# Kernel optimization log

Hardware: AMD Instinct MI355X
Metric: run time of the kernel (lower is better)

The kernel has to match this reference:

```python
import jax, jax.numpy as jnp
import numpy as np

NUM_USERS, NUM_ITEMS, D = 100000, 200000, 128
B, LLEN, SLEN = 4096, 200, 50
NEG = -1e9


def setup_inputs() -> dict:
    key = jax.random.key(0)
    ks = jax.random.split(key, 10)
    w_range = float(np.sqrt(3.0 / D))
    return {
        "user_table": 0.01 * jax.random.normal(ks[0], (NUM_USERS, D), dtype=jnp.float32),
        "item_table": 0.01 * jax.random.normal(ks[1], (NUM_ITEMS, D), dtype=jnp.float32),
        "W1": jax.random.uniform(ks[2], (2 * D, 16), minval=-w_range, maxval=w_range, dtype=jnp.float32),
        "b1": jnp.zeros((16,), dtype=jnp.float32),
        "W2": jax.random.uniform(ks[3], (16, 1), minval=-w_range, maxval=w_range, dtype=jnp.float32),
        "b2": jnp.zeros((1,), dtype=jnp.float32),
        "user_inputs": jax.random.randint(ks[4], (B,), 0, NUM_USERS, dtype=jnp.int64) if jax.config.jax_enable_x64 else jax.random.randint(ks[4], (B,), 0, NUM_USERS, dtype=jnp.int32),
        "L_inputs": jax.random.randint(ks[5], (B, LLEN), 0, NUM_ITEMS, dtype=jnp.int32),
        "S_inputs": jax.random.randint(ks[6], (B, SLEN), 0, NUM_ITEMS, dtype=jnp.int32),
        "item_inputs": jax.random.randint(ks[7], (B,), 0, NUM_ITEMS, dtype=jnp.int32),
    }


def reference(user_table, item_table, W1, b1, W2, b2,
              user_inputs, L_inputs, S_inputs, item_inputs):
    def att_logits(x):  # x: [..., 2D] -> [...]
        h = jax.nn.relu(x @ W1 + b1)
        return (h @ W2 + b2)[..., 0]

    def masked_softmax(logits, mask):  # softmax over last axis restricted to mask
        logits = jnp.where(mask, logits, NEG)
        return jax.nn.softmax(logits, axis=-1)

    u_emb = user_table[user_inputs]                      # [B, D]

    # ---- long-term attention over L history ----
    L_mask = L_inputs >= 0                               # [B, L]
    L_idx = jnp.where(L_mask, L_inputs, 0)
    L_emb = item_table[L_idx]                            # [B, L, D]
    uL = jnp.concatenate([jnp.broadcast_to(u_emb[:, None, :], L_emb.shape), L_emb], axis=-1)  # [B, L, 2D]
    w1 = masked_softmax(att_logits(uL), L_mask)          # [B, L]
    u_long = jnp.einsum('bl,bld->bd', w1, L_emb)         # [B, D]

    # ---- short-term attention over [u_long] + S (L assumed nonempty) ----
    S_mask = S_inputs >= 0                               # [B, S]
    S_idx = jnp.where(S_mask, S_inputs, 0)
    S_emb = item_table[S_idx]                            # [B, S, D]
    seq = jnp.concatenate([u_long[:, None, :], S_emb], axis=1)   # [B, 1+S, D]
    seq_mask = jnp.concatenate([jnp.ones((seq.shape[0], 1), dtype=bool), S_mask], axis=1)
    uSeq = jnp.concatenate([jnp.broadcast_to(u_emb[:, None, :], seq.shape), seq], axis=-1)  # [B, 1+S, 2D]
    w2 = masked_softmax(att_logits(uSeq), seq_mask)      # [B, 1+S]
    user_hybrid = jnp.einsum('bs,bsd->bd', w2, seq)      # [B, D]

    # ---- score: bmm([B,1,D], [B,D,1]) -> [B,1,1] ----
    item_emb = item_table[item_inputs]                   # [B, D]
    score = jnp.sum(user_hybrid * item_emb, axis=-1)[:, None, None]
    return score
```

## Files before the change

kernel.cpp:

```cpp
#include <hip/hip_runtime.h>
#include <math.h>

#define D 128
#define LLEN 200
#define SLEN 50
#define CH 64
#define ESTR 129
#define NEG (-1e9f)

__device__ __forceinline__ float wave_red_sum(float v) {
#pragma unroll
  for (int m = 32; m >= 1; m >>= 1) v += __shfl_xor(v, m, 64);
  return v;
}
__device__ __forceinline__ float block_sum(float v, float* red) {
  v = wave_red_sum(v);
  if ((threadIdx.x & 63) == 0) red[threadIdx.x >> 6] = v;
  __syncthreads();
  v = red[0] + red[1] + red[2] + red[3];
  __syncthreads();
  return v;
}

__global__ void __launch_bounds__(256, 4) din_kernel(
    const float* __restrict__ user_table, const float* __restrict__ item_table,
    const float* __restrict__ W1, const float* __restrict__ b1,
    const float* __restrict__ W2, const float* __restrict__ b2,
    const int* __restrict__ user_inputs, const int* __restrict__ L_inputs,
    const int* __restrict__ S_inputs, const int* __restrict__ item_inputs,
    float* __restrict__ out) {
  __shared__ float ebuf[CH * ESTR];
  __shared__ float hspart[4 * 65];
  __shared__ float w_sh[CH];
  __shared__ int rows1[LLEN];
  __shared__ int rowsS[SLEN];
  __shared__ float upart_sh[16];
  __shared__ float red_sh[4];

  const int b = blockIdx.x;
  const int tid = threadIdx.x;
  const int lane = tid & 63;
  const int w = __builtin_amdgcn_readfirstlane(tid >> 6);
  const int dd = tid & 127, dg = tid >> 7;
  const float4* it4 = reinterpret_cast<const float4*>(item_table);

  float* u_sh = &ebuf[0];
  float* part = &ebuf[128];
  if (tid < D) u_sh[tid] = user_table[(size_t)user_inputs[b] * D + tid];
  if (tid < LLEN) rows1[tid] = L_inputs[(size_t)b * LLEN + tid];
  if (tid < SLEN) rowsS[tid] = S_inputs[(size_t)b * SLEN + tid];
  __syncthreads();

  {
    int j = tid & 15, g = tid >> 4;
    float p = 0.f;
#pragma unroll
    for (int t = 0; t < 8; ++t) {
      int d = g * 8 + t;
      p = fmaf(u_sh[d], W1[d * 16 + j], p);
    }
    part[tid] = p;
  }
  __syncthreads();
  if (tid < 16) {
    float s = b1[tid];
#pragma unroll
    for (int g = 0; g < 16; ++g) s += part[g * 16 + tid];
    upart_sh[tid] = s;
  }
  __syncthreads();

  const float b2v = b2[0];
  const float w2a = W2[4 * w + 0], w2b = W2[4 * w + 1];
  const float w2c = W2[4 * w + 2], w2d = W2[4 * w + 3];

  float pacc = 0.f;
  float uacc = 0.f;

  for (int c = 0; c < 4; ++c) {
    const int base = c * CH;
    const int cnt = (base + CH <= LLEN) ? CH : (LLEN - base);
    const int nslot = cnt * 32;

    {
      float4 v[8];
#pragma unroll
      for (int it = 0; it < 8; ++it) {
        int s = tid + it * 256;
        if (s < nslot) {
          int gid = rows1[base + (s >> 5)];
          if (gid < 0) gid = 0;
          v[it] = it4[(size_t)gid * 32 + (s & 31)];
        }
      }
#pragma unroll
      for (int it = 0; it < 8; ++it) {
        int s = tid + it * 256;
        if (s < nslot) {
          float* dst = &ebuf[(s >> 5) * ESTR + 4 * (s & 31)];
          dst[0] = v[it].x; dst[1] = v[it].y; dst[2] = v[it].z; dst[3] = v[it].w;
        }
      }
    }
    __syncthreads();

    if (lane < cnt) {
      float a0 = 0.f, a1 = 0.f, a2 = 0.f, a3 = 0.f;
      const float* er = &ebuf[lane * ESTR];
      const float* wc = &W1[(size_t)D * 16 + 4 * w];
#pragma unroll 16
      for (int d = 0; d < D; ++d) {
        float e = er[d];
        const float* wr = wc + d * 16;
        a0 = fmaf(e, wr[0], a0);
        a1 = fmaf(e, wr[1], a1);
        a2 = fmaf(e, wr[2], a2);
        a3 = fmaf(e, wr[3], a3);
      }
      float hs = fmaxf(upart_sh[4 * w + 0] + a0, 0.f) * w2a;
      hs = fmaf(fmaxf(upart_sh[4 * w + 1] + a1, 0.f), w2b, hs);
      hs = fmaf(fmaxf(upart_sh[4 * w + 2] + a2, 0.f), w2c, hs);
      hs = fmaf(fmaxf(upart_sh[4 * w + 3] + a3, 0.f), w2d, hs);
      hspart[w * 65 + lane] = hs;
    }
    __syncthreads();

    if (tid < cnt) {
      float lg = hspart[tid] + hspart[65 + tid] + hspart[130 + tid] +
                 hspart[195 + tid] + b2v;
      float p = (rows1[base + tid] >= 0) ? expf(lg) : 0.f;
      w_sh[tid] = p;
      pacc += p;
    }
    __syncthreads();

    for (int l = dg; l < cnt; l += 2)
      uacc = fmaf(w_sh[l], ebuf[l * ESTR + dd], uacc);
    __syncthreads();
  }

  const float invS1 = 1.f / block_sum(pacc, red_sh);
  float* part2 = &ebuf[60 * ESTR];
  part2[tid] = uacc;
  __syncthreads();
  if (tid < D) {
    float ul = (part2[tid] + part2[tid + D]) * invS1;
    ebuf[tid] = ul;
  }
  __syncthreads();

  {
    const int nslot = SLEN * 32;
    float4 v[7];
#pragma unroll
    for (int it = 0; it < 7; ++it) {
      int s = tid + it * 256;
      if (s < nslot) {
        int gid = rowsS[s >> 5];
        if (gid < 0) gid = 0;
        v[it] = it4[(size_t)gid * 32 + (s & 31)];
      }
    }
#pragma unroll
    for (int it = 0; it < 7; ++it) {
      int s = tid + it * 256;
      if (s < nslot) {
        float* dst = &ebuf[((s >> 5) + 1) * ESTR + 4 * (s & 31)];
        dst[0] = v[it].x; dst[1] = v[it].y; dst[2] = v[it].z; dst[3] = v[it].w;
      }
    }
  }
  __syncthreads();

  const int n2 = 1 + SLEN;
  if (lane < n2) {
    float a0 = 0.f, a1 = 0.f, a2 = 0.f, a3 = 0.f;
    const float* er = &ebuf[lane * ESTR];
    const float* wc = &W1[(size_t)D * 16 + 4 * w];
#pragma unroll 16
    for (int d = 0; d < D; ++d) {
      float e = er[d];
      const float* wr = wc + d * 16;
      a0 = fmaf(e, wr[0], a0);
      a1 = fmaf(e, wr[1], a1);
      a2 = fmaf(e, wr[2], a2);
      a3 = fmaf(e, wr[3], a3);
    }
    float hs = fmaxf(upart_sh[4 * w + 0] + a0, 0.f) * w2a;
    hs = fmaf(fmaxf(upart_sh[4 * w + 1] + a1, 0.f), w2b, hs);
    hs = fmaf(fmaxf(upart_sh[4 * w + 2] + a2, 0.f), w2c, hs);
    hs = fmaf(fmaxf(upart_sh[4 * w + 3] + a3, 0.f), w2d, hs);
    hspart[w * 65 + lane] = hs;
  }
  __syncthreads();

  float p2 = 0.f;
  if (tid < n2) {
    float lg = hspart[tid] + hspart[65 + tid] + hspart[130 + tid] +
               hspart[195 + tid] + b2v;
    bool valid = (tid == 0) || (rowsS[tid - 1] >= 0);
    p2 = valid ? expf(lg) : 0.f;
    w_sh[tid] = p2;
  }
  const float invS2 = 1.f / block_sum(p2, red_sh);

  float uacc2 = 0.f;
  for (int l = dg; l < n2; l += 2)
    uacc2 = fmaf(w_sh[l], ebuf[l * ESTR + dd], uacc2);
  part2[tid] = uacc2;
  __syncthreads();

  float sv = 0.f;
  if (tid < D) {
    float uh = (part2[tid] + part2[tid + D]) * invS2;
    sv = uh * item_table[(size_t)item_inputs[b] * D + tid];
  }
  float tot = block_sum(sv, red_sh);
  if (tid == 0) out[b] = tot;
}

extern "C" void kernel_launch(void* const* d_in, const int* in_sizes, int n_in,
                              void* d_out, int out_size, void* d_ws, size_t ws_size,
                              hipStream_t stream) {
  const float* user_table = (const float*)d_in[0];
  const float* item_table = (const float*)d_in[1];
  const float* W1 = (const float*)d_in[2];
  const float* b1 = (const float*)d_in[3];
  const float* W2 = (const float*)d_in[4];
  const float* b2 = (const float*)d_in[5];
  const int* user_inputs = (const int*)d_in[6];
  const int* L_inputs = (const int*)d_in[7];
  const int* S_inputs = (const int*)d_in[8];
  const int* item_inputs = (const int*)d_in[9];
  float* out = (float*)d_out;

  const int B = in_sizes[6];
  din_kernel<<<B, 256, 0, stream>>>(user_table, item_table, W1, b1, W2, b2,
                                    user_inputs, L_inputs, S_inputs, item_inputs,
                                    out);
}
```

Baseline: 294.9 us.

## Prefetch next history chunk into registers and vectorize LDS access with float4

The gather of each 64-row chunk of the long history is now issued before the weighted-sum phase of the previous chunk, and the short-sequence gather is issued before the first softmax reduction. The goal is to hide global gather latency behind compute. The row stride is padded to 132 so rows are 16-byte aligned in shared memory, which lets LDS stores, the MLP dot products and the weighted sums all use float4 accesses. The weighted sum also moves from 2 to 8 row groups, with an 8-way final reduction. In exchange the kernel keeps 32 extra VGPRs of prefetched data live, which may hurt occupancy under the 256x4 launch bound, and the padded stride may change bank-conflict behaviour.

```diff
diff --git a/kernel.cpp b/kernel.cpp
--- a/kernel.cpp
+++ b/kernel.cpp
@@ -5,7 +5,7 @@
 #define LLEN 200
 #define SLEN 50
 #define CH 64
-#define ESTR 129
+#define ESTR 132
 #define NEG (-1e9f)
 
 __device__ __forceinline__ float wave_red_sum(float v) {
@@ -41,7 +41,8 @@
   const int tid = threadIdx.x;
   const int lane = tid & 63;
   const int w = __builtin_amdgcn_readfirstlane(tid >> 6);
-  const int dd = tid & 127, dg = tid >> 7;
+  const int col4 = tid & 31;
+  const int grp  = tid >> 5;
   const float4* it4 = reinterpret_cast<const float4*>(item_table);
 
   float* u_sh = &ebuf[0];
@@ -51,6 +52,23 @@
   if (tid < SLEN) rowsS[tid] = S_inputs[(size_t)b * SLEN + tid];
   __syncthreads();
 
+  auto load_chunk = [&](float4 (&v)[8], int c) {
+    const int base = c * CH;
+    const int cnt = (base + CH <= LLEN) ? CH : (LLEN - base);
+    const int nslot = cnt * 32;
+#pragma unroll
+    for (int it = 0; it < 8; ++it) {
+      int s = tid + it * 256;
+      if (s < nslot) {
+        int gid = rows1[base + (s >> 5)];
+        if (gid < 0) gid = 0;
+        v[it] = it4[(size_t)gid * 32 + (s & 31)];
+      }
+    }
+  };
+  float4 v[8];
+  load_chunk(v, 0);
+
   {
     int j = tid & 15, g = tid >> 4;
     float p = 0.f;
@@ -75,47 +93,37 @@
   const float w2c = W2[4 * w + 2], w2d = W2[4 * w + 3];
 
   float pacc = 0.f;
-  float uacc = 0.f;
+  float4 uacc = make_float4(0.f, 0.f, 0.f, 0.f);
 
   for (int c = 0; c < 4; ++c) {
     const int base = c * CH;
     const int cnt = (base + CH <= LLEN) ? CH : (LLEN - base);
     const int nslot = cnt * 32;
 
-    {
-      float4 v[8];
-#pragma unroll
-      for (int it = 0; it < 8; ++it) {
-        int s = tid + it * 256;
-        if (s < nslot) {
-          int gid = rows1[base + (s >> 5)];
-          if (gid < 0) gid = 0;
-          v[it] = it4[(size_t)gid * 32 + (s & 31)];
-        }
-      }
-#pragma unroll
-      for (int it = 0; it < 8; ++it) {
-        int s = tid + it * 256;
-        if (s < nslot) {
-          float* dst = &ebuf[(s >> 5) * ESTR + 4 * (s & 31)];
-          dst[0] = v[it].x; dst[1] = v[it].y; dst[2] = v[it].z; dst[3] = v[it].w;
-        }
-      }
+#pragma unroll
+    for (int it = 0; it < 8; ++it) {
+      int s = tid + it * 256;
+      if (s < nslot)
+        reinterpret_cast<float4*>(&ebuf[(s >> 5) * ESTR])[s & 31] = v[it];
     }
     __syncthreads();
 
     if (lane < cnt) {
       float a0 = 0.f, a1 = 0.f, a2 = 0.f, a3 = 0.f;
-      const float* er = &ebuf[lane * ESTR];
+      const float4* er4 = reinterpret_cast<const float4*>(&ebuf[lane * ESTR]);
       const float* wc = &W1[(size_t)D * 16 + 4 * w];
-#pragma unroll 16
-      for (int d = 0; d < D; ++d) {
-        float e = er[d];
-        const float* wr = wc + d * 16;
-        a0 = fmaf(e, wr[0], a0);
-        a1 = fmaf(e, wr[1], a1);
-        a2 = fmaf(e, wr[2], a2);
-        a3 = fmaf(e, wr[3], a3);
+#pragma unroll 8
+      for (int k = 0; k < 32; ++k) {
+        float4 e = er4[k];
+        const float* wr = wc + k * 64;
+        a0 = fmaf(e.x, wr[0],  a0); a1 = fmaf(e.x, wr[1],  a1);
+        a2 = fmaf(e.x, wr[2],  a2); a3 = fmaf(e.x, wr[3],  a3);
+        a0 = fmaf(e.y, wr[16], a0); a1 = fmaf(e.y, wr[17], a1);
+        a2 = fmaf(e.y, wr[18], a2); a3 = fmaf(e.y, wr[19], a3);
+        a0 = fmaf(e.z, wr[32], a0); a1 = fmaf(e.z, wr[33], a1);
+        a2 = fmaf(e.z, wr[34], a2); a3 = fmaf(e.z, wr[35], a3);
+        a0 = fmaf(e.w, wr[48], a0); a1 = fmaf(e.w, wr[49], a1);
+        a2 = fmaf(e.w, wr[50], a2); a3 = fmaf(e.w, wr[51], a3);
       }
       float hs = fmaxf(upart_sh[4 * w + 0] + a0, 0.f) * w2a;
       hs = fmaf(fmaxf(upart_sh[4 * w + 1] + a1, 0.f), w2b, hs);
@@ -134,57 +142,65 @@
     }
     __syncthreads();
 
-    for (int l = dg; l < cnt; l += 2)
-      uacc = fmaf(w_sh[l], ebuf[l * ESTR + dd], uacc);
-    __syncthreads();
+    if (c < 3) load_chunk(v, c + 1);
+
+    for (int l = grp; l < cnt; l += 8) {
+      float wl = w_sh[l];
+      const float4 e = reinterpret_cast<const float4*>(&ebuf[l * ESTR])[col4];
+      uacc.x = fmaf(wl, e.x, uacc.x);
+      uacc.y = fmaf(wl, e.y, uacc.y);
+      uacc.z = fmaf(wl, e.z, uacc.z);
+      uacc.w = fmaf(wl, e.w, uacc.w);
+    }
+    __syncthreads();
+  }
+
+  float4 v2[7];
+#pragma unroll
+  for (int it = 0; it < 7; ++it) {
+    int s = tid + it * 256;
+    if (s < SLEN * 32) {
+      int gid = rowsS[s >> 5];
+      if (gid < 0) gid = 0;
+      v2[it] = it4[(size_t)gid * 32 + (s & 31)];
+    }
   }
 
   const float invS1 = 1.f / block_sum(pacc, red_sh);
-  float* part2 = &ebuf[60 * ESTR];
-  part2[tid] = uacc;
+  float* scr = &ebuf[52 * ESTR];
+  reinterpret_cast<float4*>(scr)[tid] = uacc;
   __syncthreads();
   if (tid < D) {
-    float ul = (part2[tid] + part2[tid + D]) * invS1;
-    ebuf[tid] = ul;
-  }
-  __syncthreads();
-
-  {
-    const int nslot = SLEN * 32;
-    float4 v[7];
-#pragma unroll
-    for (int it = 0; it < 7; ++it) {
-      int s = tid + it * 256;
-      if (s < nslot) {
-        int gid = rowsS[s >> 5];
-        if (gid < 0) gid = 0;
-        v[it] = it4[(size_t)gid * 32 + (s & 31)];
-      }
-    }
-#pragma unroll
-    for (int it = 0; it < 7; ++it) {
-      int s = tid + it * 256;
-      if (s < nslot) {
-        float* dst = &ebuf[((s >> 5) + 1) * ESTR + 4 * (s & 31)];
-        dst[0] = v[it].x; dst[1] = v[it].y; dst[2] = v[it].z; dst[3] = v[it].w;
-      }
-    }
+    float s = 0.f;
+#pragma unroll
+    for (int g = 0; g < 8; ++g) s += scr[g * 128 + tid];
+    ebuf[tid] = s * invS1;
+  }
+#pragma unroll
+  for (int it = 0; it < 7; ++it) {
+    int s = tid + it * 256;
+    if (s < SLEN * 32)
+      reinterpret_cast<float4*>(&ebuf[((s >> 5) + 1) * ESTR])[s & 31] = v2[it];
   }
   __syncthreads();
 
   const int n2 = 1 + SLEN;
   if (lane < n2) {
     float a0 = 0.f, a1 = 0.f, a2 = 0.f, a3 = 0.f;
-    const float* er = &ebuf[lane * ESTR];
+    const float4* er4 = reinterpret_cast<const float4*>(&ebuf[lane * ESTR]);
     const float* wc = &W1[(size_t)D * 16 + 4 * w];
-#pragma unroll 16
-    for (int d = 0; d < D; ++d) {
-      float e = er[d];
-      const float* wr = wc + d * 16;
-      a0 = fmaf(e, wr[0], a0);
-      a1 = fmaf(e, wr[1], a1);
-      a2 = fmaf(e, wr[2], a2);
-      a3 = fmaf(e, wr[3], a3);
+#pragma unroll 8
+    for (int k = 0; k < 32; ++k) {
+      float4 e = er4[k];
+      const float* wr = wc + k * 64;
+      a0 = fmaf(e.x, wr[0],  a0); a1 = fmaf(e.x, wr[1],  a1);
+      a2 = fmaf(e.x, wr[2],  a2); a3 = fmaf(e.x, wr[3],  a3);
+      a0 = fmaf(e.y, wr[16], a0); a1 = fmaf(e.y, wr[17], a1);
+      a2 = fmaf(e.y, wr[18], a2); a3 = fmaf(e.y, wr[19], a3);
+      a0 = fmaf(e.z, wr[32], a0); a1 = fmaf(e.z, wr[33], a1);
+      a2 = fmaf(e.z, wr[34], a2); a3 = fmaf(e.z, wr[35], a3);
+      a0 = fmaf(e.w, wr[48], a0); a1 = fmaf(e.w, wr[49], a1);
+      a2 = fmaf(e.w, wr[50], a2); a3 = fmaf(e.w, wr[51], a3);
     }
     float hs = fmaxf(upart_sh[4 * w + 0] + a0, 0.f) * w2a;
     hs = fmaf(fmaxf(upart_sh[4 * w + 1] + a1, 0.f), w2b, hs);
@@ -204,15 +220,24 @@
   }
   const float invS2 = 1.f / block_sum(p2, red_sh);
 
-  float uacc2 = 0.f;
-  for (int l = dg; l < n2; l += 2)
-    uacc2 = fmaf(w_sh[l], ebuf[l * ESTR + dd], uacc2);
-  part2[tid] = uacc2;
+  float4 uacc2 = make_float4(0.f, 0.f, 0.f, 0.f);
+  for (int l = grp; l < n2; l += 8) {
+    float wl = w_sh[l];
+    const float4 e = reinterpret_cast<const float4*>(&ebuf[l * ESTR])[col4];
+    uacc2.x = fmaf(wl, e.x, uacc2.x);
+    uacc2.y = fmaf(wl, e.y, uacc2.y);
+    uacc2.z = fmaf(wl, e.z, uacc2.z);
+    uacc2.w = fmaf(wl, e.w, uacc2.w);
+  }
+  reinterpret_cast<float4*>(scr)[tid] = uacc2;
   __syncthreads();
 
   float sv = 0.f;
   if (tid < D) {
-    float uh = (part2[tid] + part2[tid + D]) * invS2;
+    float s = 0.f;
+#pragma unroll
+    for (int g = 0; g < 8; ++g) s += scr[g * 128 + tid];
+    float uh = s * invS2;
     sv = uh * item_table[(size_t)item_inputs[b] * D + tid];
   }
   float tot = block_sum(sv, red_sh);
```

New measurement: 474.4 us. +60.9%, slower.
